# Optimization experiments

Hardware: AMD Instinct MI355X
Metric: run time of the kernel (lower is better)

Reference implementation:

```python
import jax, jax.numpy as jnp
import numpy as np

NUM_NODES = 100000
NUM_EDGES = 3200000
N_PER = 400            # nodes per graph (equal-size graphs)
NUM_GRAPHS = 250
K = 100                # sort-pooling k
DIM = 32
IN_DIM = 128
TOTAL = 3 * DIM + 1    # 97 = concat channel count
GDIM = 128
OUT_DIM = 2
DENSE_DIM = (((K - 2) // 2 + 1) - 5 + 1) * 64  # 46*64 = 2944


def setup_inputs() -> dict:
    key = jax.random.key(0)
    ks = jax.random.split(key, 12)

    def lin(k, shape, fan_in):
        return jax.random.normal(k, shape, jnp.float32) / np.float32(np.sqrt(fan_in))

    return {
        "x": jax.random.normal(ks[0], (NUM_NODES, IN_DIM), jnp.float32),
        "edge_index": jax.random.randint(ks[1], (2, NUM_EDGES), 0, NUM_NODES, dtype=jnp.int32),
        "batch": jnp.arange(NUM_NODES, dtype=jnp.int32) // N_PER,
        "W1": lin(ks[2], (IN_DIM, DIM), IN_DIM), "b1": jnp.zeros((DIM,), jnp.float32),
        "W2": lin(ks[3], (DIM, DIM), DIM),       "b2": jnp.zeros((DIM,), jnp.float32),
        "W3": lin(ks[4], (DIM, DIM), DIM),       "b3": jnp.zeros((DIM,), jnp.float32),
        "W4": lin(ks[5], (DIM, 1), DIM),         "b4": jnp.zeros((1,), jnp.float32),
        "cw1": lin(ks[6], (128, 1, TOTAL), TOTAL),   "cb1": jnp.zeros((128,), jnp.float32),
        "cw2": lin(ks[7], (64, 128, 5), 128 * 5),    "cb2": jnp.zeros((64,), jnp.float32),
        "fw1": lin(ks[8], (GDIM, DENSE_DIM), DENSE_DIM), "fb1": jnp.zeros((GDIM,), jnp.float32),
        "fw3": lin(ks[9], (OUT_DIM, GDIM), GDIM),        "fb3": jnp.zeros((OUT_DIM,), jnp.float32),
    }


def _gcn(h_in, W, b, src, dst, coef, deg_inv):
    # GCNConv (improved=False): D^{-1/2}(A+I)D^{-1/2} (h W) + b
    h = h_in @ W
    agg = jax.ops.segment_sum(h[src] * coef, dst, num_segments=NUM_NODES)
    return agg + h * deg_inv[:, None] + b  # deg_inv = self-loop norm dis[i]^2


def reference(x, edge_index, batch, W1, b1, W2, b2, W3, b3, W4, b4,
              cw1, cb1, cw2, cb2, fw1, fb1, fw3, fb3):
    src, dst = edge_index[0], edge_index[1]
    deg = jax.ops.segment_sum(jnp.ones((NUM_EDGES,), x.dtype), dst, num_segments=NUM_NODES) + 1.0
    dis = jax.lax.rsqrt(deg)
    coef = (dis[src] * dis[dst])[:, None]
    deg_inv = 1.0 / deg

    x1 = jnp.tanh(_gcn(x,  W1, b1, src, dst, coef, deg_inv))
    x2 = jnp.tanh(_gcn(x1, W2, b2, src, dst, coef, deg_inv))
    x3 = jnp.tanh(_gcn(x2, W3, b3, src, dst, coef, deg_inv))
    x4 = jnp.tanh(_gcn(x2, W4, b4, src, dst, coef, deg_inv))  # NB: conv4 consumes x2 (as in source)
    xc = jnp.concatenate([x1, x2, x3, x4], axis=1)  # [N, 97]

    # global_sort_pool: per-graph descending sort by last channel, keep top K nodes
    order = jnp.lexsort((-xc[:, -1], batch))  # primary: graph id, secondary: -last channel
    xs = xc[order].reshape(NUM_GRAPHS, N_PER, TOTAL)[:, :K]  # [B, K, 97]

    # Conv1d(1, 128, kernel=stride=97) over flattened [B,1,K*97] == per-slot linear map
    c1 = jax.nn.relu(jnp.einsum('bkt,ct->bck', xs, cw1[:, 0, :]) + cb1[None, :, None])  # [B,128,K]
    p1 = c1.reshape(NUM_GRAPHS, 128, K // 2, 2).max(axis=-1)  # MaxPool1d(2,2) -> [B,128,50]
    c2 = jax.lax.conv_general_dilated(p1, cw2, (1,), 'VALID',
                                      dimension_numbers=('NCH', 'OIH', 'NCH'))
    c2 = jax.nn.relu(c2 + cb2[None, :, None])  # [B,64,46]

    flat = c2.reshape(NUM_GRAPHS, -1)            # [B, 2944]
    h = jax.nn.relu(flat @ fw1.T + fb1)          # fc1 + relu (dropout = identity in eval)
    logits = h @ fw3.T + fb3                     # fc3
    return jax.nn.log_softmax(logits, axis=-1)
```

## Files before the change

### kernel.cpp

```cpp
#include <hip/hip_runtime.h>
#include <hip/hip_bf16.h>

#define NNODES 100000
#define NEDGES 3200000
#define NPADE  4000000
#define NPER   400
#define NGRAPH 250
#define KTOP   100
#define DIM    32
#define INDIM  128
#define TOTALC 97
#define BSHIFT 7
#define BNODES 128
#define NBUCK  782
#define NCHUNK 200
#define CHSZ   16000

__device__ __forceinline__ float bf(unsigned short u) {
    return __uint_as_float(((unsigned)u) << 16);
}
__device__ __forceinline__ unsigned short f2bf(float f) {
    unsigned u = __float_as_uint(f);
    unsigned r = ((u >> 16) & 1u) + 0x7FFFu;
    return (unsigned short)((u + r) >> 16);
}

#define OW_W1   0
#define OW_B1   4096
#define OW_W2   4128
#define OW_B2   5152
#define OW_W3   5184
#define OW_B3   6208
#define OW_W4   6240
#define OW_B4   6272
#define OW_CW1  6280
#define OW_CB1  18696
#define OW_CW2  18824
#define OW_CB2  59784
#define OW_FW1  59848
#define OW_FB1  436680
#define OW_FW3  436808
#define OW_FB3  437064
#define OW_TOT  437072

struct Srcs { const void* p[16]; };

__global__ void k_setup(const unsigned int* __restrict__ xw, Srcs sr,
                        float* __restrict__ dst, float* __restrict__ fw1t,
                        float* __restrict__ w2t8, int* __restrict__ flag,
                        float* __restrict__ hb, float* __restrict__ x1b,
                        float* __restrict__ x2b, float* __restrict__ h4b) {
    __shared__ int cs[256];
    int t = threadIdx.x;
    int c = 0;
    for (int i = t; i < 4096; i += 256) {
        unsigned e = (xw[i] >> 23) & 0xFFu;
        if (e >= 100u && e <= 150u) c++;
    }
    cs[t] = c;
    __syncthreads();
    for (int off = 128; off > 0; off >>= 1) {
        if (t < off) cs[t] += cs[t + off];
        __syncthreads();
    }
    int isb = (cs[0] < 2048) ? 1 : 0;
    if (blockIdx.x == 0) {
        if (t == 0) flag[0] = isb;
        if (t < 32) {
            hb[(size_t)NNODES * DIM + t]  = 0.f;
            x1b[(size_t)NNODES * DIM + t] = 0.f;
            x2b[(size_t)NNODES * DIM + t] = 0.f;
        }
        if (t == 32) h4b[NNODES] = 0.f;
    }
    long idx = (long)blockIdx.x * 256 + t;
    if (idx < OW_TOT) {
        const int st[16] = {OW_W1, OW_B1, OW_W2, OW_B2, OW_W3, OW_B3, OW_W4, OW_B4,
                            OW_CW1, OW_CB1, OW_CW2, OW_CB2, OW_FW1, OW_FB1, OW_FW3, OW_FB3};
        const int nn[16] = {4096, 32, 1024, 32, 1024, 32, 32, 1,
                            12416, 128, 40960, 64, 376832, 128, 256, 2};
        #pragma unroll
        for (int s = 0; s < 16; s++) {
            if (idx >= st[s] && idx < st[s] + nn[s]) {
                int l = (int)idx - st[s];
                dst[idx] = isb ? bf(((const unsigned short*)sr.p[s])[l])
                               : ((const float*)sr.p[s])[l];
            }
        }
    } else if (idx < OW_TOT + 376832) {
        int i2 = (int)(idx - OW_TOT);
        float v = isb ? bf(((const unsigned short*)sr.p[12])[i2])
                      : ((const float*)sr.p[12])[i2];
        int j = i2 / 2944, d = i2 - j * 2944;
        fw1t[d * 128 + j] = v;
    } else if (idx < OW_TOT + 376832 + 65536) {
        int k = (int)(idx - OW_TOT - 376832);
        int q = k & 7;
        int co = k >> 3;
        int cc = co >> 6, o = co & 63;
        float v = 0.f;
        if (q < 5) {
            int si = (o * 128 + cc) * 5 + q;
            v = isb ? bf(((const unsigned short*)sr.p[10])[si])
                    : ((const float*)sr.p[10])[si];
        }
        w2t8[k] = v;
    }
}


__global__ __launch_bounds__(1024) void k_hist(const int* __restrict__ ei, int* __restrict__ ghist) {
    __shared__ int h[NBUCK];
    int c = blockIdx.x, t = threadIdx.x;
    for (int i = t; i < NBUCK; i += 1024) h[i] = 0;
    __syncthreads();
    int base = c * CHSZ;
    for (int e = base + t; e < base + CHSZ; e += 1024)
        atomicAdd(&h[ei[NEDGES + e] >> BSHIFT], 1);
    __syncthreads();
    for (int i = t; i < NBUCK; i += 1024) ghist[i * NCHUNK + c] = h[i];
}

__global__ __launch_bounds__(256) void k_scanChunk(int* __restrict__ ghist, int* __restrict__ bcnt) {
    __shared__ int s[256];
    int b = blockIdx.x, t = threadIdx.x;
    int v = (t < NCHUNK) ? ghist[b * NCHUNK + t] : 0;
    s[t] = v;
    __syncthreads();
    for (int o = 1; o < 256; o <<= 1) {
        int u = (t >= o) ? s[t - o] : 0;
        __syncthreads();
        s[t] += u;
        __syncthreads();
    }
    if (t < NCHUNK) ghist[b * NCHUNK + t] = s[t] - v;
    if (t == NCHUNK - 1) bcnt[b] = s[t];
}

__global__ void k_scanB(const int* __restrict__ in, int* __restrict__ out) {
    __shared__ int s[1024];
    int t = threadIdx.x;
    int v = (t < NBUCK) ? in[t] : 0;
    s[t] = v;
    __syncthreads();
    for (int o = 1; o < 1024; o <<= 1) {
        int u = (t >= o) ? s[t - o] : 0;
        __syncthreads();
        s[t] += u;
        __syncthreads();
    }
    if (t < NBUCK) out[t] = s[t] - v;
}

__global__ __launch_bounds__(1024) void k_binwrite(const int* __restrict__ ei, const int* __restrict__ boff,
                           const int* __restrict__ ghist, unsigned* __restrict__ staged) {
    __shared__ int cur[NBUCK];
    int c = blockIdx.x, t = threadIdx.x;
    for (int i = t; i < NBUCK; i += 1024) cur[i] = boff[i] + ghist[i * NCHUNK + c];
    __syncthreads();
    int base = c * CHSZ;
    for (int e = base + t; e < base + CHSZ; e += 1024) {
        int s = ei[e], d = ei[NEDGES + e];
        int b = d >> BSHIFT;
        int pos = atomicAdd(&cur[b], 1);
        staged[pos] = ((unsigned)(d & (BNODES - 1)) << 17) | (unsigned)s;
    }
}

__global__ __launch_bounds__(256) void k_nodecnt(const unsigned* __restrict__ staged,
                          const int* __restrict__ boff, int* __restrict__ degi,
                          float* __restrict__ dis, float* __restrict__ rdis,
                          int* __restrict__ bucksum) {
    __shared__ int cnt[BNODES];
    __shared__ int ps[256];
    int b = blockIdx.x, t = threadIdx.x;
    if (t < BNODES) cnt[t] = 0;
    __syncthreads();
    int s0 = boff[b];
    int s1 = (b + 1 < NBUCK) ? boff[b + 1] : NEDGES;
    for (int i = s0 + t; i < s1; i += 256)
        atomicAdd(&cnt[staged[i] >> 17], 1);
    __syncthreads();
    int n0 = b << BSHIFT;
    int nn = min(BNODES, NNODES - n0);
    int dg = (t < nn) ? cnt[t] : 0;
    if (t < nn) {
        degi[n0 + t] = dg;
        float d = (float)(dg + 1);
        dis[n0 + t]  = rsqrtf(d);
        rdis[n0 + t] = sqrtf(d);
    }
    ps[t] = (t < nn) ? ((dg + 7) & ~7) : 0;
    __syncthreads();
    for (int off = 128; off > 0; off >>= 1) {
        if (t < off) ps[t] += ps[t + off];
        __syncthreads();
    }
    if (t == 0) bucksum[b] = ps[0];
}

__global__ __launch_bounds__(256) void k_csrfix(const unsigned* __restrict__ staged,
                         const int* __restrict__ boff, const int* __restrict__ buckoff,
                         const int* __restrict__ degi,
                         int* __restrict__ csr_src, int* __restrict__ row_off) {
    __shared__ int cnt[BNODES];
    __shared__ int sc[BNODES];
    __shared__ int rofs[BNODES];
    int b = blockIdx.x, t = threadIdx.x;
    int n0 = b << BSHIFT;
    int nn = min(BNODES, NNODES - n0);
    int pd = (t < nn) ? ((degi[n0 + t] + 7) & ~7) : 0;
    if (t < BNODES) { cnt[t] = 0; sc[t] = pd; }
    __syncthreads();
    for (int o = 1; o < BNODES; o <<= 1) {
        int u = (t >= o && t < BNODES) ? sc[t - o] : 0;
        __syncthreads();
        if (t < BNODES) sc[t] += u;
        __syncthreads();
    }
    if (t < BNODES) rofs[t] = buckoff[b] + sc[t] - pd;
    if (t < nn) row_off[n0 + t] = rofs[t];
    __syncthreads();
    int s0 = boff[b];
    int s1 = (b + 1 < NBUCK) ? boff[b + 1] : NEDGES;
    for (int i = s0 + t; i < s1; i += 256) {
        unsigned rec = staged[i];
        int dl = rec >> 17, s = rec & 0x1FFFF;
        int r = atomicAdd(&cnt[dl], 1);
        csr_src[rofs[dl] + r] = s;
    }
    __syncthreads();
    if (t < nn) {
        int d = cnt[t], dp = (d + 7) & ~7;
        for (int s2 = d; s2 < dp; s2++) csr_src[rofs[t] + s2] = NNODES;
    }
}


__global__ void k_mm1(const void* __restrict__ xraw, const float* __restrict__ W1f,
                      const int* __restrict__ flag, const float* __restrict__ dis,
                      float* __restrict__ h) {
    __shared__ float w[INDIM * DIM];
    __shared__ float xsh[8 * INDIM];
    int t = threadIdx.x;
    for (int i = t; i < INDIM * DIM; i += 256) w[i] = W1f[i];
    if (flag[0]) {
        const unsigned int* xsrc = (const unsigned int*)((const unsigned short*)xraw
                                   + (size_t)blockIdx.x * 8 * INDIM);
        for (int i = t; i < 512; i += 256) {
            unsigned u = xsrc[i];
            xsh[2 * i]     = __uint_as_float(u << 16);
            xsh[2 * i + 1] = __uint_as_float(u & 0xFFFF0000u);
        }
    } else {
        const float4* xsrc = (const float4*)((const float*)xraw + (size_t)blockIdx.x * 8 * INDIM);
        float4* xdst = (float4*)xsh;
        for (int i = t; i < 256; i += 256) xdst[i] = xsrc[i];
    }
    __syncthreads();
    int ln = t >> 5, c = t & 31;
    const float* xr = xsh + ln * INDIM;
    float acc = 0.f;
    #pragma unroll 8
    for (int j = 0; j < INDIM; j++) acc += xr[j] * w[j * DIM + c];
    int node = blockIdx.x * 8 + ln;
    h[(size_t)node * DIM + c] = acc * dis[node];
}

__global__ void k_gather(const float* __restrict__ xin, const float* __restrict__ h4s,
                         const int* __restrict__ csr_src,
                         const int* __restrict__ row_off, const int* __restrict__ degi,
                         const float* __restrict__ dis,
                         const float* __restrict__ Wm,
                         const float* __restrict__ bias,
                         const float* __restrict__ w4v,
                         const float* __restrict__ b4,
                         float* __restrict__ xout, float* __restrict__ x4out,
                         float* __restrict__ h4out, int scaleOut) {
    __shared__ float wsh[DIM * DIM];
    __shared__ float w4sh[DIM];
    __shared__ float zsh[8 * DIM];
    __shared__ float osh[8 * DIM];
    int t = threadIdx.x;
    if (Wm)  for (int i = t; i < DIM * DIM; i += 256) wsh[i] = Wm[i];
    if (w4v && t < DIM) w4sh[t] = w4v[t];
    int node = blockIdx.x * 8 + (t >> 5);
    int lane = t & 31;
    int wg   = t >> 5;
    int start = row_off[node];
    int cnt   = degi[node];
    int iters = (cnt + 7) >> 3;
    const int4* ip = (const int4*)(csr_src + start);
    float acc0 = 0.f, acc1 = 0.f;
    if (iters > 0) {
        int4 iA = ip[0], iB = ip[1];
        for (int k = 1; k < iters; k++) {
            int4 nA = ip[2 * k], nB = ip[2 * k + 1];
            acc0 += xin[(size_t)iA.x * DIM + lane];
            acc1 += xin[(size_t)iA.y * DIM + lane];
            acc0 += xin[(size_t)iA.z * DIM + lane];
            acc1 += xin[(size_t)iA.w * DIM + lane];
            acc0 += xin[(size_t)iB.x * DIM + lane];
            acc1 += xin[(size_t)iB.y * DIM + lane];
            acc0 += xin[(size_t)iB.z * DIM + lane];
            acc1 += xin[(size_t)iB.w * DIM + lane];
            iA = nA; iB = nB;
        }
        acc0 += xin[(size_t)iA.x * DIM + lane];
        acc1 += xin[(size_t)iA.y * DIM + lane];
        acc0 += xin[(size_t)iA.z * DIM + lane];
        acc1 += xin[(size_t)iA.w * DIM + lane];
        acc0 += xin[(size_t)iB.x * DIM + lane];
        acc1 += xin[(size_t)iB.y * DIM + lane];
        acc0 += xin[(size_t)iB.z * DIM + lane];
        acc1 += xin[(size_t)iB.w * DIM + lane];
    }
    float disv = dis[node];
    float z = (acc0 + acc1 + xin[(size_t)node * DIM + lane]) * disv;
    if (!Wm) {
        float outv = tanhf(z + bias[lane]);
        xout[(size_t)node * DIM + lane] = outv * disv;
    } else {
        zsh[wg * DIM + lane] = z;
        __syncthreads();
        const float* zr = zsh + wg * DIM;
        float a = bias[lane];
        #pragma unroll
        for (int j = 0; j < DIM; j++) a += zr[j] * wsh[j * DIM + lane];
        float outv = tanhf(a);
        xout[(size_t)node * DIM + lane] = scaleOut ? outv * disv : outv;
        if (h4out) {
            osh[wg * DIM + lane] = outv;
            __syncthreads();
            if (lane == 0) {
                const float* xr = osh + wg * DIM;
                float a4 = 0.f;
                #pragma unroll
                for (int j = 0; j < DIM; j++) a4 += xr[j] * w4sh[j];
                h4out[node] = a4 * disv;
            }
        }
    }
    if (h4s) {
        int cntp = iters << 3;
        float a4 = 0.f;
        for (int ee = lane; ee < cntp; ee += 32)
            a4 += h4s[csr_src[start + ee]];
        for (int off = 16; off > 0; off >>= 1) a4 += __shfl_xor(a4, off, 32);
        if (lane == 0) x4out[node] = tanhf((a4 + h4s[node]) * disv + b4[0]);
    }
}

__global__ __launch_bounds__(1024) void
k_sortconv1(const float* __restrict__ x1, const float* __restrict__ x2,
            const float* __restrict__ x3, const float* __restrict__ x4,
            const float* __restrict__ rdis,
            const float* __restrict__ cw1f, const float* __restrict__ cb1f,
            float* __restrict__ p1g) {
    __shared__ unsigned long long keys[512];
    __shared__ __align__(16) float xs[32 * 100];
    __shared__ __align__(16) float ws[32 * 128];
    __shared__ int nsh[KTOP];
    __shared__ float rdl[KTOP];
    int g = blockIdx.x, t = threadIdx.x;
    for (int i = t; i < 512; i += 1024) {
        unsigned long long kk = 0xFFFFFFFFFFFFFFFFULL;
        if (i < NPER) {
            unsigned u = __float_as_uint(x4[g * NPER + i]);
            u = (u & 0x80000000u) ? ~u : (u | 0x80000000u);
            kk = ((unsigned long long)(~u) << 32) | (unsigned)i;
        }
        keys[i] = kk;
    }
    __syncthreads();
    for (int k = 2; k <= 512; k <<= 1)
        for (int j = k >> 1; j > 0; j >>= 1) {
            for (int i = t; i < 512; i += 1024) {
                int l = i ^ j;
                if (l > i) {
                    unsigned long long a = keys[i], b = keys[l];
                    bool asc = ((i & k) == 0);
                    if ((a > b) == asc) { keys[i] = b; keys[l] = a; }
                }
            }
            __syncthreads();
        }
    if (t < KTOP) {
        int nid = g * NPER + (int)(unsigned)(keys[t] & 0xFFFFFFFFu);
        nsh[t] = nid;
        rdl[t] = rdis[nid];
    }
    int ct = (t & 31) * 4;
    int kt = (t >> 5) * 4;
    bool act = (t < 800);
    float acc[4][4] = {};
    for (int ch = 0; ch < 3; ch++) {
        const float* arr = (ch == 0) ? x1 : (ch == 1) ? x2 : x3;
        __syncthreads();
        for (int i = t; i < 3200; i += 1024) {
            int q = i & 31, k = i >> 5;
            float v = arr[(size_t)nsh[k] * 32 + q];
            if (ch < 2) v *= rdl[k];
            xs[q * 100 + k] = v;
        }
        for (int i = t; i < 4096; i += 1024) {
            int c = i & 127, q = i >> 7;
            ws[q * 128 + c] = cw1f[c * TOTALC + ch * 32 + q];
        }
        __syncthreads();
        if (act) {
            for (int q = 0; q < 32; q++) {
                float4 wv = *(const float4*)&ws[q * 128 + ct];
                float4 xv = *(const float4*)&xs[q * 100 + kt];
                float xa[4] = { xv.x, xv.y, xv.z, xv.w };
                float wa[4] = { wv.x, wv.y, wv.z, wv.w };
                #pragma unroll
                for (int a = 0; a < 4; a++)
                    #pragma unroll
                    for (int b = 0; b < 4; b++)
                        acc[a][b] += xa[a] * wa[b];
            }
        }
    }
    if (act) {
        float wa[4];
        #pragma unroll
        for (int b = 0; b < 4; b++) wa[b] = cw1f[(ct + b) * TOTALC + 96];
        #pragma unroll
        for (int a = 0; a < 4; a++) {
            float xv = x4[nsh[kt + a]];
            #pragma unroll
            for (int b = 0; b < 4; b++) acc[a][b] += xv * wa[b];
        }
        int jbase = kt >> 1;
        #pragma unroll
        for (int b = 0; b < 4; b++) {
            float bias = cb1f[ct + b];
            float m0 = fmaxf(fmaxf(acc[0][b], acc[1][b]) + bias, 0.f);
            float m1 = fmaxf(fmaxf(acc[2][b], acc[3][b]) + bias, 0.f);
            p1g[((size_t)g * 128 + ct + b) * 50 + jbase]     = m0;
            p1g[((size_t)g * 128 + ct + b) * 50 + jbase + 1] = m1;
        }
    }
}

__global__ __launch_bounds__(512) void
k_conv2(const float* __restrict__ p1g, const float* __restrict__ w2t8,
        const float* __restrict__ cb2f, float* __restrict__ flatg) {
    __shared__ __align__(16) float p1s[128 * 52];
    __shared__ float fl[64 * 25];
    int bid = blockIdx.x;
    int g = bid >> 1, ph = bid & 1;
    int t = threadIdx.x;
    int p0 = ph ? 24 : 0;
    int np = ph ? 22 : 24;
    for (int i = t; i < 128 * 50; i += 512) {
        int c = i / 50, p = i % 50;
        p1s[c * 52 + p] = p1g[(size_t)g * 6400 + i];
    }
    for (int i = t; i < 128 * 2; i += 512) {
        int c = i >> 1;
        p1s[c * 52 + 50 + (i & 1)] = 0.f;
    }
    for (int i = t; i < 64 * 25; i += 512) fl[i] = 0.f;
    __syncthreads();
    {
        int o = t & 63;
        int c8 = t >> 6;
        float acc[24];
        #pragma unroll
        for (int p = 0; p < 24; p++) acc[p] = 0.f;
        int cbeg = c8 * 16;
        for (int c = cbeg; c < cbeg + 16; c++) {
            const float4* wb = (const float4*)(w2t8 + (((size_t)c * 64 + o) << 3));
            float4 wA = wb[0], wB = wb[1];
            float w0 = wA.x, w1 = wA.y, w2 = wA.z, w3 = wA.w, w4 = wB.x;
            float win[28];
            const float4* wsrc = (const float4*)&p1s[c * 52 + p0];
            #pragma unroll
            for (int v = 0; v < 7; v++) {
                float4 f = wsrc[v];
                win[4 * v] = f.x; win[4 * v + 1] = f.y; win[4 * v + 2] = f.z; win[4 * v + 3] = f.w;
            }
            #pragma unroll
            for (int p = 0; p < 24; p++)
                acc[p] += win[p] * w0 + win[p + 1] * w1 + win[p + 2] * w2
                        + win[p + 3] * w3 + win[p + 4] * w4;
        }
        for (int p = 0; p < np; p++) atomicAdd(&fl[o * 25 + p], acc[p]);
    }
    __syncthreads();
    for (int i = t; i < 64 * 24; i += 512) {
        int o = i / 24, p = i - o * 24;
        if (p < np)
            flatg[(size_t)g * 2944 + o * 46 + p0 + p] = fmaxf(fl[o * 25 + p] + cb2f[o], 0.f);
    }
}

__global__ __launch_bounds__(1024) void
k_fc1(const float* __restrict__ flatg, const float* __restrict__ fw1t,
      float* __restrict__ hpart) {
    __shared__ float fls[5 * 368];
    __shared__ float hp[8 * 5 * 128];
    int b = blockIdx.x;
    int gt = b >> 3, kt = b & 7;
    int t = threadIdx.x;
    int g0 = gt * 5;
    int d0 = kt * 368;
    for (int i = t; i < 5 * 368; i += 1024) {
        int g = i / 368, dd = i - g * 368;
        fls[i] = flatg[(size_t)(g0 + g) * 2944 + d0 + dd];
    }
    __syncthreads();
    int og = t & 127, s8 = t >> 7;
    int ds = s8 * 46;
    const float* wp = fw1t + (size_t)(d0 + ds) * 128 + og;
    const float* f0 = fls + ds;
    float a0 = 0.f, a1 = 0.f, a2 = 0.f, a3 = 0.f, a4 = 0.f;
    #pragma unroll 2
    for (int d = 0; d < 46; d++) {
        float w = wp[(size_t)d * 128];
        a0 += f0[d]            * w;
        a1 += f0[368 + d]      * w;
        a2 += f0[2 * 368 + d]  * w;
        a3 += f0[3 * 368 + d]  * w;
        a4 += f0[4 * 368 + d]  * w;
    }
    hp[(s8 * 5 + 0) * 128 + og] = a0;
    hp[(s8 * 5 + 1) * 128 + og] = a1;
    hp[(s8 * 5 + 2) * 128 + og] = a2;
    hp[(s8 * 5 + 3) * 128 + og] = a3;
    hp[(s8 * 5 + 4) * 128 + og] = a4;
    __syncthreads();
    if (t < 640) {
        int g = t >> 7, o2 = t & 127;
        float s = 0.f;
        #pragma unroll
        for (int s2 = 0; s2 < 8; s2++) s += hp[(s2 * 5 + g) * 128 + o2];
        hpart[((size_t)kt * NGRAPH + g0 + g) * 128 + o2] = s;
    }
}

__global__ void k_fc3(const float* __restrict__ hpart, const float* __restrict__ fb1f,
                      const float* __restrict__ fw3f, const float* __restrict__ fb3f,
                      const int* __restrict__ flag, void* __restrict__ outp) {
    __shared__ float hsh[128];
    int g = blockIdx.x, t = threadIdx.x;
    float s = fb1f[t];
    #pragma unroll
    for (int kt = 0; kt < 8; kt++) s += hpart[((size_t)kt * NGRAPH + g) * 128 + t];
    hsh[t] = fmaxf(s, 0.f);
    __syncthreads();
    if (t < 64) {
        float h0 = hsh[t], h1 = hsh[t + 64];
        float l0 = h0 * fw3f[t] + h1 * fw3f[t + 64];
        float l1 = h0 * fw3f[128 + t] + h1 * fw3f[192 + t];
        #pragma unroll
        for (int off = 32; off > 0; off >>= 1) {
            l0 += __shfl_down(l0, off, 64);
            l1 += __shfl_down(l1, off, 64);
        }
        if (t == 0) {
            l0 += fb3f[0]; l1 += fb3f[1];
            float m = fmaxf(l0, l1);
            float lse = m + logf(expf(l0 - m) + expf(l1 - m));
            if (flag[0]) {
                unsigned short* ob = (unsigned short*)outp;
                ob[g * 2 + 0] = f2bf(l0 - lse);
                ob[g * 2 + 1] = f2bf(l1 - lse);
            } else {
                float* of = (float*)outp;
                of[g * 2 + 0] = l0 - lse;
                of[g * 2 + 1] = l1 - lse;
            }
        }
    }
}


extern "C" void kernel_launch(void* const* d_in, const int* in_sizes, int n_in,
                              void* d_out, int out_size, void* d_ws, size_t ws_size,
                              hipStream_t stream) {
    const void* x  = d_in[0];
    const int* ei  = (const int*)d_in[1];

    char* p = (char*)d_ws;
    auto alloc = [&](size_t bytes) -> void* {
        void* r = (void*)p;
        p += (bytes + 255) & ~(size_t)255;
        return r;
    };
    int*      flag    = (int*)alloc(256);
    float*    wcv     = (float*)alloc((size_t)OW_TOT * 4);
    float*    fw1t    = (float*)alloc((size_t)376832 * 4);
    int*      ghist   = (int*)alloc((size_t)NBUCK * NCHUNK * 4);
    int*      bcnt    = (int*)alloc(1024 * 4);
    int*      boff    = (int*)alloc(1024 * 4);
    int*      bucksum = (int*)alloc(1024 * 4);
    int*      buckoff = (int*)alloc(1024 * 4);
    int*      degi    = (int*)alloc((size_t)NNODES * 4);
    int*      row_off = (int*)alloc((size_t)NNODES * 4);
    float*    dis     = (float*)alloc((size_t)NNODES * 4);
    float*    rdis    = (float*)alloc((size_t)NNODES * 4);
    unsigned* staged  = (unsigned*)alloc((size_t)NEDGES * 4);
    int*      csr_src = (int*)alloc((size_t)NPADE * 4);
    float*    hbuf    = (float*)alloc(((size_t)NNODES * DIM + 256) * 4);
    float*    h4buf   = (float*)alloc(((size_t)NNODES + 256) * 4);
    float*    x1      = (float*)alloc(((size_t)NNODES * DIM + 256) * 4);
    float*    x2      = (float*)alloc(((size_t)NNODES * DIM + 256) * 4);
    float*    x3      = (float*)alloc((size_t)NNODES * DIM * 4);
    float*    x4      = (float*)alloc((size_t)NNODES * 4);
    float*    p1g     = (float*)alloc((size_t)NGRAPH * 128 * 50 * 4);
    float*    w2t     = (float*)alloc((size_t)64 * 128 * 8 * 4);
    float*    flatg   = (float*)alloc((size_t)NGRAPH * 2944 * 4);
    float*    hpart   = (float*)alloc((size_t)8 * NGRAPH * 128 * 4);
    (void)in_sizes; (void)n_in; (void)out_size; (void)ws_size;

    Srcs sr;
    for (int i = 0; i < 16; i++) sr.p[i] = d_in[3 + i];
    k_setup<<<3436, 256, 0, stream>>>((const unsigned int*)x, sr, wcv, fw1t, w2t, flag,
                                      hbuf, x1, x2, h4buf);

    k_hist     <<<NCHUNK, 1024, 0, stream>>>(ei, ghist);
    k_scanChunk<<<NBUCK, 256, 0, stream>>>(ghist, bcnt);
    k_scanB    <<<1, 1024, 0, stream>>>(bcnt, boff);
    k_binwrite <<<NCHUNK, 1024, 0, stream>>>(ei, boff, ghist, staged);
    k_nodecnt  <<<NBUCK, 256, 0, stream>>>(staged, boff, degi, dis, rdis, bucksum);
    k_scanB    <<<1, 1024, 0, stream>>>(bucksum, buckoff);
    k_csrfix   <<<NBUCK, 256, 0, stream>>>(staged, boff, buckoff, degi, csr_src, row_off);

    k_mm1   <<<12500, 256, 0, stream>>>(x, wcv + OW_W1, flag, dis, hbuf);
    k_gather<<<12500, 256, 0, stream>>>(hbuf, nullptr, csr_src, row_off, degi, dis,
                                        nullptr, wcv + OW_B1, nullptr, nullptr,
                                        x1, nullptr, nullptr, 1);
    k_gather<<<12500, 256, 0, stream>>>(x1, nullptr, csr_src, row_off, degi, dis,
                                        wcv + OW_W2, wcv + OW_B2, wcv + OW_W4, nullptr,
                                        x2, nullptr, h4buf, 1);
    k_gather<<<12500, 256, 0, stream>>>(x2, h4buf, csr_src, row_off, degi, dis,
                                        wcv + OW_W3, wcv + OW_B3, nullptr, wcv + OW_B4,
                                        x3, x4, nullptr, 0);

    k_sortconv1<<<NGRAPH, 1024, 0, stream>>>(x1, x2, x3, x4, rdis,
                                             wcv + OW_CW1, wcv + OW_CB1, p1g);
    k_conv2    <<<2 * NGRAPH, 512, 0, stream>>>(p1g, w2t, wcv + OW_CB2, flatg);
    k_fc1      <<<400, 1024, 0, stream>>>(flatg, fw1t, hpart);
    k_fc3      <<<NGRAPH, 128, 0, stream>>>(hpart, wcv + OW_FB1, wcv + OW_FW3, wcv + OW_FB3,
                                            flag, d_out);
}
```

Before: 525.8 us.

## Replace histogram-scan binning with fixed-capacity buckets and atomic cursors

Edge binning by destination bucket now uses fixed-capacity slots per bucket (8192 entries) with a global atomic cursor per bucket. This folds the histogram, two scans and the bin-write pass into one scatter kernel. The prefix over bucket sums is computed inside k_csrfix by reducing the preceding buckets, so a separate scan launch is dropped. It relies on no bucket holding more than 8192 edges; uniform random edges average about 4096 per bucket, but a skewed graph would overflow. Edge order within a bucket also becomes nondeterministic.

```diff
diff --git a/kernel.cpp b/kernel.cpp
--- a/kernel.cpp
+++ b/kernel.cpp
@@ -15,6 +15,7 @@
 #define NBUCK  782
 #define NCHUNK 200
 #define CHSZ   16000
+#define BCAP   8192
 
 __device__ __forceinline__ float bf(unsigned short u) {
     return __uint_as_float(((unsigned)u) << 16);
@@ -49,7 +50,8 @@
                         float* __restrict__ dst, float* __restrict__ fw1t,
                         float* __restrict__ w2t8, int* __restrict__ flag,
                         float* __restrict__ hb, float* __restrict__ x1b,
-                        float* __restrict__ x2b, float* __restrict__ h4b) {
+                        float* __restrict__ x2b, float* __restrict__ h4b,
+                        int* __restrict__ gcur) {
     __shared__ int cs[256];
     int t = threadIdx.x;
     int c = 0;
@@ -72,6 +74,7 @@
             x2b[(size_t)NNODES * DIM + t] = 0.f;
         }
         if (t == 32) h4b[NNODES] = 0.f;
+        for (int i = t; i < NBUCK; i += 256) gcur[i] = i * BCAP;
     }
     long idx = (long)blockIdx.x * 256 + t;
     if (idx < OW_TOT) {
@@ -108,9 +111,11 @@
     }
 }
 
-
-__global__ __launch_bounds__(1024) void k_hist(const int* __restrict__ ei, int* __restrict__ ghist) {
+__global__ __launch_bounds__(1024) void
+k_scatter(const int* __restrict__ ei, int* __restrict__ gcur,
+          unsigned* __restrict__ staged) {
     __shared__ int h[NBUCK];
+    __shared__ int cur[NBUCK];
     int c = blockIdx.x, t = threadIdx.x;
     for (int i = t; i < NBUCK; i += 1024) h[i] = 0;
     __syncthreads();
@@ -118,47 +123,11 @@
     for (int e = base + t; e < base + CHSZ; e += 1024)
         atomicAdd(&h[ei[NEDGES + e] >> BSHIFT], 1);
     __syncthreads();
-    for (int i = t; i < NBUCK; i += 1024) ghist[i * NCHUNK + c] = h[i];
-}
-
-__global__ __launch_bounds__(256) void k_scanChunk(int* __restrict__ ghist, int* __restrict__ bcnt) {
-    __shared__ int s[256];
-    int b = blockIdx.x, t = threadIdx.x;
-    int v = (t < NCHUNK) ? ghist[b * NCHUNK + t] : 0;
-    s[t] = v;
-    __syncthreads();
-    for (int o = 1; o < 256; o <<= 1) {
-        int u = (t >= o) ? s[t - o] : 0;
-        __syncthreads();
-        s[t] += u;
-        __syncthreads();
-    }
-    if (t < NCHUNK) ghist[b * NCHUNK + t] = s[t] - v;
-    if (t == NCHUNK - 1) bcnt[b] = s[t];
-}
-
-__global__ void k_scanB(const int* __restrict__ in, int* __restrict__ out) {
-    __shared__ int s[1024];
-    int t = threadIdx.x;
-    int v = (t < NBUCK) ? in[t] : 0;
-    s[t] = v;
-    __syncthreads();
-    for (int o = 1; o < 1024; o <<= 1) {
-        int u = (t >= o) ? s[t - o] : 0;
-        __syncthreads();
-        s[t] += u;
-        __syncthreads();
-    }
-    if (t < NBUCK) out[t] = s[t] - v;
-}
-
-__global__ __launch_bounds__(1024) void k_binwrite(const int* __restrict__ ei, const int* __restrict__ boff,
-                           const int* __restrict__ ghist, unsigned* __restrict__ staged) {
-    __shared__ int cur[NBUCK];
-    int c = blockIdx.x, t = threadIdx.x;
-    for (int i = t; i < NBUCK; i += 1024) cur[i] = boff[i] + ghist[i * NCHUNK + c];
-    __syncthreads();
-    int base = c * CHSZ;
+    for (int i = t; i < NBUCK; i += 1024) {
+        int n = h[i];
+        cur[i] = n ? atomicAdd(&gcur[i], n) : 0;
+    }
+    __syncthreads();
     for (int e = base + t; e < base + CHSZ; e += 1024) {
         int s = ei[e], d = ei[NEDGES + e];
         int b = d >> BSHIFT;
@@ -168,7 +137,7 @@
 }
 
 __global__ __launch_bounds__(256) void k_nodecnt(const unsigned* __restrict__ staged,
-                          const int* __restrict__ boff, int* __restrict__ degi,
+                          const int* __restrict__ gcur, int* __restrict__ degi,
                           float* __restrict__ dis, float* __restrict__ rdis,
                           int* __restrict__ bucksum) {
     __shared__ int cnt[BNODES];
@@ -176,8 +145,8 @@
     int b = blockIdx.x, t = threadIdx.x;
     if (t < BNODES) cnt[t] = 0;
     __syncthreads();
-    int s0 = boff[b];
-    int s1 = (b + 1 < NBUCK) ? boff[b + 1] : NEDGES;
+    int s0 = b * BCAP;
+    int s1 = gcur[b];
     for (int i = s0 + t; i < s1; i += 256)
         atomicAdd(&cnt[staged[i] >> 17], 1);
     __syncthreads();
@@ -200,13 +169,24 @@
 }
 
 __global__ __launch_bounds__(256) void k_csrfix(const unsigned* __restrict__ staged,
-                         const int* __restrict__ boff, const int* __restrict__ buckoff,
+                         const int* __restrict__ gcur, const int* __restrict__ bucksum,
                          const int* __restrict__ degi,
                          int* __restrict__ csr_src, int* __restrict__ row_off) {
     __shared__ int cnt[BNODES];
     __shared__ int sc[BNODES];
     __shared__ int rofs[BNODES];
+    __shared__ int red[256];
     int b = blockIdx.x, t = threadIdx.x;
+    int acc = 0;
+    for (int i = t; i < b; i += 256) acc += bucksum[i];
+    red[t] = acc;
+    __syncthreads();
+    for (int off = 128; off > 0; off >>= 1) {
+        if (t < off) red[t] += red[t + off];
+        __syncthreads();
+    }
+    int bko = red[0];
+    __syncthreads();
     int n0 = b << BSHIFT;
     int nn = min(BNODES, NNODES - n0);
     int pd = (t < nn) ? ((degi[n0 + t] + 7) & ~7) : 0;
@@ -218,11 +198,11 @@
         if (t < BNODES) sc[t] += u;
         __syncthreads();
     }
-    if (t < BNODES) rofs[t] = buckoff[b] + sc[t] - pd;
+    if (t < BNODES) rofs[t] = bko + sc[t] - pd;
     if (t < nn) row_off[n0 + t] = rofs[t];
     __syncthreads();
-    int s0 = boff[b];
-    int s1 = (b + 1 < NBUCK) ? boff[b + 1] : NEDGES;
+    int s0 = b * BCAP;
+    int s1 = gcur[b];
     for (int i = s0 + t; i < s1; i += 256) {
         unsigned rec = staged[i];
         int dl = rec >> 17, s = rec & 0x1FFFF;
@@ -593,16 +573,13 @@
     int*      flag    = (int*)alloc(256);
     float*    wcv     = (float*)alloc((size_t)OW_TOT * 4);
     float*    fw1t    = (float*)alloc((size_t)376832 * 4);
-    int*      ghist   = (int*)alloc((size_t)NBUCK * NCHUNK * 4);
-    int*      bcnt    = (int*)alloc(1024 * 4);
-    int*      boff    = (int*)alloc(1024 * 4);
+    int*      gcur    = (int*)alloc(1024 * 4);
     int*      bucksum = (int*)alloc(1024 * 4);
-    int*      buckoff = (int*)alloc(1024 * 4);
     int*      degi    = (int*)alloc((size_t)NNODES * 4);
     int*      row_off = (int*)alloc((size_t)NNODES * 4);
     float*    dis     = (float*)alloc((size_t)NNODES * 4);
     float*    rdis    = (float*)alloc((size_t)NNODES * 4);
-    unsigned* staged  = (unsigned*)alloc((size_t)NEDGES * 4);
+    unsigned* staged  = (unsigned*)alloc((size_t)NBUCK * BCAP * 4);
     int*      csr_src = (int*)alloc((size_t)NPADE * 4);
     float*    hbuf    = (float*)alloc(((size_t)NNODES * DIM + 256) * 4);
     float*    h4buf   = (float*)alloc(((size_t)NNODES + 256) * 4);
@@ -619,15 +596,11 @@
     Srcs sr;
     for (int i = 0; i < 16; i++) sr.p[i] = d_in[3 + i];
     k_setup<<<3436, 256, 0, stream>>>((const unsigned int*)x, sr, wcv, fw1t, w2t, flag,
-                                      hbuf, x1, x2, h4buf);
-
-    k_hist     <<<NCHUNK, 1024, 0, stream>>>(ei, ghist);
-    k_scanChunk<<<NBUCK, 256, 0, stream>>>(ghist, bcnt);
-    k_scanB    <<<1, 1024, 0, stream>>>(bcnt, boff);
-    k_binwrite <<<NCHUNK, 1024, 0, stream>>>(ei, boff, ghist, staged);
-    k_nodecnt  <<<NBUCK, 256, 0, stream>>>(staged, boff, degi, dis, rdis, bucksum);
-    k_scanB    <<<1, 1024, 0, stream>>>(bucksum, buckoff);
-    k_csrfix   <<<NBUCK, 256, 0, stream>>>(staged, boff, buckoff, degi, csr_src, row_off);
+                                      hbuf, x1, x2, h4buf, gcur);
+
+    k_scatter<<<NCHUNK, 1024, 0, stream>>>(ei, gcur, staged);
+    k_nodecnt<<<NBUCK, 256, 0, stream>>>(staged, gcur, degi, dis, rdis, bucksum);
+    k_csrfix <<<NBUCK, 256, 0, stream>>>(staged, gcur, bucksum, degi, csr_src, row_off);
 
     k_mm1   <<<12500, 256, 0, stream>>>(x, wcv + OW_W1, flag, dis, hbuf);
     k_gather<<<12500, 256, 0, stream>>>(hbuf, nullptr, csr_src, row_off, degi, dis,
```

After: 516.6 us. Within noise of the previous version (-1.8%).
